# Kernel optimization log

Hardware: AMD Instinct MI355X
Metric: run time of the kernel (lower is better)

The kernel has to match this reference:

```python
import jax, jax.numpy as jnp
import numpy as np

BN_EPS = 1e-5
MIN_LENGTH = 10
HIDDEN = 256


def _conv(x, w, stride):
    # x: [N,C,H,W], w: [O,I,3,3], SAME-ish padding 1
    return jax.lax.conv_general_dilated(
        x, w, (stride, stride), [(1, 1), (1, 1)],
        dimension_numbers=("NCHW", "OIHW", "NCHW"))


def _bn_relu(x, g, b, m, v):
    # eval-mode BatchNorm2d followed by ReLU, folded into scale/shift
    inv = g / jnp.sqrt(v + BN_EPS)
    return jax.nn.relu(x * inv[None, :, None, None] + (b - m * inv)[None, :, None, None])


def setup_inputs() -> dict:
    key = jax.random.key(0)
    ks = jax.random.split(key, 16)
    B, S, C, H, W = 16, 64, 3, 64, 64
    d = {"imgs": jax.random.normal(ks[0], (B, S, C, H, W), dtype=jnp.float32)}
    # conv stack: (out_ch, in_ch, stride)
    specs = [(16, 3, 2), (16, 16, 1), (32, 16, 2), (32, 32, 1), (64, 32, 2), (64, 64, 1)]
    for i, (o, ic, _s) in enumerate(specs):
        d[f"w{i}"] = jax.random.normal(ks[1 + i], (o, ic, 3, 3), dtype=jnp.float32) * 0.05
        d[f"g{i}"] = jnp.ones((o,), jnp.float32)
        d[f"b{i}"] = jnp.zeros((o,), jnp.float32)
        d[f"m{i}"] = jnp.zeros((o,), jnp.float32)
        d[f"v{i}"] = jnp.ones((o,), jnp.float32)
    in_dim = 64 * 8 * 8  # plane3 * 8 * 8
    d["w_ih"] = jax.random.normal(ks[8], (4 * HIDDEN, in_dim), dtype=jnp.float32) * 0.02
    d["w_hh"] = jax.random.normal(ks[9], (4 * HIDDEN, HIDDEN), dtype=jnp.float32) * 0.05
    d["b_ih"] = jnp.zeros((4 * HIDDEN,), jnp.float32)
    d["b_hh"] = jnp.zeros((4 * HIDDEN,), jnp.float32)
    d["cls_w"] = jax.random.normal(ks[10], (1, HIDDEN), dtype=jnp.float32) * 0.05
    d["cls_b"] = jnp.zeros((1,), jnp.float32)
    return d


def reference(imgs, w0, g0, b0, m0, v0, w1, g1, b1, m1, v1, w2, g2, b2, m2, v2,
              w3, g3, b3, m3, v3, w4, g4, b4, m4, v4, w5, g5, b5, m5, v5,
              w_ih, w_hh, b_ih, b_hh, cls_w, cls_b):
    B, S, C, H, W = imgs.shape
    x = imgs.reshape(B * S, C, H, W)
    layers = [(w0, g0, b0, m0, v0, 2), (w1, g1, b1, m1, v1, 1),
              (w2, g2, b2, m2, v2, 2), (w3, g3, b3, m3, v3, 1),
              (w4, g4, b4, m4, v4, 2), (w5, g5, b5, m5, v5, 1)]
    for w, g, b, m, v, s in layers:
        x = _bn_relu(_conv(x, w, s), g, b, m, v)
    # [B*S, 64, 8, 8] -> [S, B, 4096]
    feats = x.reshape(B, S, -1).transpose(1, 0, 2)

    def step(carry, x_t):
        h, c = carry
        gates = x_t @ w_ih.T + b_ih + h @ w_hh.T + b_hh
        i, f, g, o = jnp.split(gates, 4, axis=-1)
        c = jax.nn.sigmoid(f) * c + jax.nn.sigmoid(i) * jnp.tanh(g)
        h = jax.nn.sigmoid(o) * jnp.tanh(c)
        return (h, c), h

    h0 = jnp.zeros((B, HIDDEN), feats.dtype)
    c0 = jnp.zeros((B, HIDDEN), feats.dtype)
    _, hs = jax.lax.scan(step, (h0, c0), feats)  # [S, B, 256]
    kept = hs[MIN_LENGTH + 1:]                    # [S-11, B, 256]
    out = jnp.tanh(kept @ cls_w.T + cls_b)        # [S-11, B, 1]
    return out.transpose(1, 0, 2)                 # [B, S-11, 1]
```

## Files before the change

### kernel.cpp

```cpp
#include <hip/hip_runtime.h>
#include <cmath>


typedef __attribute__((ext_vector_type(8))) __bf16 bf16x8;
typedef __attribute__((ext_vector_type(4))) float f32x4;

__device__ __forceinline__ float sigmoidf_(float x) { return 1.f / (1.f + expf(-x)); }

__device__ __forceinline__ unsigned short f2bf(float f) {
  unsigned u = __float_as_uint(f);
  unsigned r = (u + 0x7fffu + ((u >> 16) & 1u)) >> 16;
  return (unsigned short)r;
}
__device__ __forceinline__ float bf2f(unsigned short h) {
  return __uint_as_float(((unsigned)h) << 16);
}

struct FoldPack {
  const float *w[6], *g[6], *b[6], *m[6], *v[6];
  float *wf[6], *bias[6];
  int oc[6], ic[6];
};

__global__ __launch_bounds__(256) void fold_all(FoldPack p) {
  const int layer = blockIdx.y;
  const int OC = p.oc[layer], IC = p.ic[layer];
  const int total = OC * IC * 9;
  const float* w = p.w[layer];
  float* wf = p.wf[layer];
  for (int i = blockIdx.x * 256 + threadIdx.x; i < total; i += gridDim.x * 256) {
    int oc = i / (IC * 9);
    int r  = i % (IC * 9);
    int ic = r / 9;
    int k  = r % 9;
    int ky = k / 3, kx = k % 3;
    float inv = p.g[layer][oc] / sqrtf(p.v[layer][oc] + 1e-5f);
    wf[(((ic * 3 + ky) * OC) + oc) * 4 + kx] = w[i] * inv;
  }
  if (blockIdx.x == 0) {
    int i = threadIdx.x;
    if (i < OC) {
      float inv = p.g[layer][i] / sqrtf(p.v[layer][i] + 1e-5f);
      p.bias[layer][i] = p.b[layer][i] - p.m[layer][i] * inv;
    }
  }
}

struct PackPack {
  const float *w[5], *g[5], *v[5];
  unsigned short *wh[5], *wl[5];
  int ic[5], oc[5], kg[5], kreal[5];
};

__global__ __launch_bounds__(256) void pack_w(PackPack p) {
  const int layer = blockIdx.y;
  const int IC = p.ic[layer], KG = p.kg[layer], K = p.kreal[layer];
  const int MT = p.oc[layer] / 16;
  const int total = MT * KG * 512;
  for (int i = blockIdx.x * 256 + threadIdx.x; i < total; i += gridDim.x * 256) {
    int j = i & 7;
    int lane = (i >> 3) & 63;
    int gmt = i >> 9;
    int m = (gmt / KG) * 16 + (lane & 15);
    int k = 32 * (gmt % KG) + 8 * (lane >> 4) + j;
    float val = 0.f;
    if (k < K) {
      int tap = k / IC, ic = k % IC;
      int ky = tap / 3, kx = tap % 3;
      float inv = p.g[layer][m] / sqrtf(p.v[layer][m] + 1e-5f);
      val = p.w[layer][((m * IC + ic) * 3 + ky) * 3 + kx] * inv;
    }
    unsigned short h = f2bf(val);
    p.wh[layer][i] = h;
    p.wl[layer][i] = f2bf(val - bf2f(h));
  }
}

template<int IC, int OC, int IH, int IW, int STRIDE, int TPOS, int SPLITY,
         int ICS, int MINW>
__global__ __launch_bounds__(256, MINW) void conv_bn_relu(
    const float* __restrict__ in, const float* __restrict__ wf,
    const float* __restrict__ bias, float* __restrict__ out)
{
  constexpr int OH = IH / STRIDE, OW = IW / STRIDE;
  constexpr int OHB = OH / SPLITY;
  constexpr int RIH = (SPLITY == 1) ? (IH + 2) : ((OHB - 1) * STRIDE + 3);
  constexpr int PIW = IW + 4;
  constexpr int PLANE = RIH * PIW;
  constexpr int NPOS = OHB * OW;
  constexpr int WPOS = NPOS / TPOS;
  constexpr int SLOT = WPOS * ICS;
  constexpr int GROUPS = 256 / SLOT;
  constexpr int TOC = OC / GROUPS;
  constexpr int CH = IC / ICS;
  constexpr int SPAN = (TPOS - 1) * STRIDE + 3;
  constexpr int NW = (SPAN + 3) / 4;
  constexpr int XSLOTS = OW / TPOS;
  static_assert(SLOT % 64 == 0 && GROUPS * SLOT == 256 && GROUPS * TOC == OC, "tiling");

  __shared__ float s_in[IC * PLANE];

  const int tid = threadIdx.x;
  const int n     = (SPLITY == 1) ? blockIdx.x : blockIdx.x / SPLITY;
  const int split = (SPLITY == 1) ? 0 : blockIdx.x % SPLITY;
  const int ry0 = split * OHB;
  const int r0  = ry0 * STRIDE - 1;

  for (int i = tid; i < IC * PLANE / 4; i += 256)
    ((float4*)s_in)[i] = float4{0.f, 0.f, 0.f, 0.f};
  __syncthreads();

  constexpr int ROWF4 = IW / 4;
  constexpr int NSTG = IC * RIH * ROWF4;
  for (int i = tid; i < NSTG; i += 256) {
    int rw  = i % ROWF4;
    int t   = i / ROWF4;
    int row = t % RIH;
    int ic  = t / RIH;
    int giy = r0 + row;
    if (giy >= 0 && giy < IH) {
      float4 v = *(const float4*)(in + ((size_t)(n * IC + ic) * IH + giy) * IW + rw * 4);
      float* dst = &s_in[(ic * RIH + row) * PIW + 1 + rw * 4];
      dst[0] = v.x; dst[1] = v.y; dst[2] = v.z; dst[3] = v.w;
    }
  }
  __syncthreads();

  const int group  = tid / SLOT;
  const int sl     = tid % SLOT;
  const int icq    = sl / WPOS;
  const int worker = sl % WPOS;
  const int oy  = worker / XSLOTS;
  const int ox0 = (worker % XSLOTS) * TPOS;
  const int xb  = ox0 * STRIDE;

  const int oc0u = __builtin_amdgcn_readfirstlane(group * TOC);
  const float4* wg = (const float4*)wf + oc0u;

  float acc[TOC][TPOS];
  #pragma unroll
  for (int a = 0; a < TOC; ++a)
    #pragma unroll
    for (int p = 0; p < TPOS; ++p) acc[a][p] = 0.f;

  for (int icl = 0; icl < CH; ++icl) {
    const int ic = icq * CH + icl;
    const float* sI = &s_in[ic * PLANE];
    #pragma unroll
    for (int ky = 0; ky < 3; ++ky) {
      float row[NW * 4];
      {
        const float4* rp = (const float4*)&sI[(oy * STRIDE + ky) * PIW + xb];
        #pragma unroll
        for (int w = 0; w < NW; ++w) {
          float4 t4 = rp[w];
          row[4*w+0] = t4.x; row[4*w+1] = t4.y;
          row[4*w+2] = t4.z; row[4*w+3] = t4.w;
        }
      }
      const float4* wrow = wg + (ic * 3 + ky) * OC;
      #pragma unroll
      for (int oc = 0; oc < TOC; ++oc) {
        float4 w4 = wrow[oc];
        #pragma unroll
        for (int p = 0; p < TPOS; ++p)
          acc[oc][p] = fmaf(row[p * STRIDE + 0], w4.x,
                       fmaf(row[p * STRIDE + 1], w4.y,
                       fmaf(row[p * STRIDE + 2], w4.z, acc[oc][p])));
      }
    }
  }

  #pragma unroll
  for (int d = WPOS; d < SLOT; d <<= 1)
    #pragma unroll
    for (int oc = 0; oc < TOC; ++oc)
      #pragma unroll
      for (int p = 0; p < TPOS; ++p)
        acc[oc][p] += __shfl_xor(acc[oc][p], d);

  if (icq == 0) {
    float* outN = out + (size_t)n * (OC * OH * OW);
    #pragma unroll
    for (int oc = 0; oc < TOC; ++oc) {
      const float bb = bias[oc0u + oc];
      float* op = outN + ((size_t)(oc0u + oc) * OH + (ry0 + oy)) * OW + ox0;
      #pragma unroll
      for (int vq = 0; vq < TPOS / 4; ++vq) {
        float4 val;
        val.x = fmaxf(acc[oc][vq*4+0] + bb, 0.f);
        val.y = fmaxf(acc[oc][vq*4+1] + bb, 0.f);
        val.z = fmaxf(acc[oc][vq*4+2] + bb, 0.f);
        val.w = fmaxf(acc[oc][vq*4+3] + bb, 0.f);
        *(float4*)(op + vq * 4) = val;
      }
    }
  }
}

template<int IC, int OC, int IH, int IW, int STRIDE, int SPLITY, int KG, int ZROW>
__global__ __launch_bounds__(256, 2) void conv_mfma(
    const float* __restrict__ in, const unsigned short* __restrict__ Ah,
    const unsigned short* __restrict__ Al, const float* __restrict__ bias,
    float* __restrict__ out)
{
  constexpr int OH = IH / STRIDE, OW = IW / STRIDE;
  constexpr int OHB = OH / SPLITY;
  constexpr int N = OHB * OW;
  constexpr int NT = N / 16;
  constexpr int NTW = NT / 4;
  constexpr int MT = OC / 16;
  constexpr int ICP = IC + 8;
  constexpr int PW = IW + 3;
  constexpr int PH = (OHB - 1) * STRIDE + 3 + ZROW;
  constexpr int SZ = ((PH * PW * ICP + 7) / 8) * 8;
  static_assert(NT % 4 == 0, "nt");

  __shared__ unsigned short s_h[SZ];
  __shared__ unsigned short s_l[SZ];

  const int tid = threadIdx.x;
  const int n     = (SPLITY == 1) ? blockIdx.x : blockIdx.x / SPLITY;
  const int split = (SPLITY == 1) ? 0 : blockIdx.x % SPLITY;
  const int y0 = split * OHB;
  const int r0 = y0 * STRIDE - 1;

  for (int i = tid * 8; i < SZ; i += 2048) {
    *(int4*)&s_h[i] = int4{0, 0, 0, 0};
    *(int4*)&s_l[i] = int4{0, 0, 0, 0};
  }
  __syncthreads();

  constexpr int ROWF4 = IW / 4;
  for (int i = tid; i < IC * PH * ROWF4; i += 256) {
    int rw  = i % ROWF4;
    int t   = i / ROWF4;
    int row = t % PH;
    int ic  = t / PH;
    int giy = r0 + row;
    if (giy >= 0 && giy < IH) {
      float4 v = *(const float4*)(in + ((size_t)(n * IC + ic) * IH + giy) * IW + rw * 4);
      int base = (row * PW + rw * 4 + 1) * ICP + ic;
      float vv[4] = {v.x, v.y, v.z, v.w};
      #pragma unroll
      for (int e = 0; e < 4; ++e) {
        unsigned short h = f2bf(vv[e]);
        s_h[base + e * ICP] = h;
        s_l[base + e * ICP] = f2bf(vv[e] - bf2f(h));
      }
    }
  }
  __syncthreads();

  const int wave = tid >> 6;
  const int lane = tid & 63;
  const int l16  = lane & 15;
  const int quad = lane >> 4;

  f32x4 acc[MT][NTW];
  #pragma unroll
  for (int mt = 0; mt < MT; ++mt)
    #pragma unroll
    for (int nt = 0; nt < NTW; ++nt) acc[mt][nt] = f32x4{0.f, 0.f, 0.f, 0.f};

  for (int g = 0; g < KG; ++g) {
    const int k0 = 32 * g + 8 * quad;
    const int tap = k0 / IC;
    const int ic0 = k0 % IC;
    const int ky = tap / 3;
    const int kx = tap - ky * 3;
    bf16x8 afh[MT], afl[MT];
    #pragma unroll
    for (int mt = 0; mt < MT; ++mt) {
      size_t wo = ((size_t)(mt * KG + g) * 64 + lane) * 8;
      afh[mt] = __builtin_bit_cast(bf16x8, *(const int4*)(Ah + wo));
      afl[mt] = __builtin_bit_cast(bf16x8, *(const int4*)(Al + wo));
    }
    #pragma unroll
    for (int nt = 0; nt < NTW; ++nt) {
      int p = (wave * NTW + nt) * 16 + l16;
      int py = p / OW, px = p % OW;
      int addr = ((py * STRIDE + ky) * PW + px * STRIDE + kx) * ICP + ic0;
      bf16x8 bh = __builtin_bit_cast(bf16x8, *(const int4*)&s_h[addr]);
      bf16x8 bl = __builtin_bit_cast(bf16x8, *(const int4*)&s_l[addr]);
      #pragma unroll
      for (int mt = 0; mt < MT; ++mt) {
        acc[mt][nt] = __builtin_amdgcn_mfma_f32_16x16x32_bf16(afh[mt], bh, acc[mt][nt], 0, 0, 0);
        acc[mt][nt] = __builtin_amdgcn_mfma_f32_16x16x32_bf16(afh[mt], bl, acc[mt][nt], 0, 0, 0);
        acc[mt][nt] = __builtin_amdgcn_mfma_f32_16x16x32_bf16(afl[mt], bh, acc[mt][nt], 0, 0, 0);
      }
    }
  }

  #pragma unroll
  for (int mt = 0; mt < MT; ++mt)
    #pragma unroll
    for (int nt = 0; nt < NTW; ++nt) {
      int p = (wave * NTW + nt) * 16 + l16;
      int py = p / OW, px = p % OW;
      #pragma unroll
      for (int r = 0; r < 4; ++r) {
        int oc = mt * 16 + quad * 4 + r;
        float v = acc[mt][nt][r] + bias[oc];
        out[((size_t)(n * OC + oc) * OH + y0 + py) * OW + px] = fmaxf(v, 0.f);
      }
    }
}

__global__ __launch_bounds__(256) void split_a(
    const float* __restrict__ feats, unsigned short* __restrict__ ah,
    unsigned short* __restrict__ al)
{
  int i4 = blockIdx.x * 256 + threadIdx.x;
  int e = i4 * 4;
  int n = e >> 12;
  int k = e & 4095;
  int r = (n & 63) * 16 + (n >> 6);
  float4 v = ((const float4*)feats)[i4];
  ushort4 h, l;
  h.x = f2bf(v.x); l.x = f2bf(v.x - bf2f(h.x));
  h.y = f2bf(v.y); l.y = f2bf(v.y - bf2f(h.y));
  h.z = f2bf(v.z); l.z = f2bf(v.z - bf2f(h.z));
  h.w = f2bf(v.w); l.w = f2bf(v.w - bf2f(h.w));
  *(ushort4*)(ah + (size_t)r * 4096 + k) = h;
  *(ushort4*)(al + (size_t)r * 4096 + k) = l;
}

__global__ __launch_bounds__(256) void split_b(
    const float* __restrict__ w_ih, unsigned short* __restrict__ bh,
    unsigned short* __restrict__ bl)
{
  int i4 = blockIdx.x * 256 + threadIdx.x;
  float4 v = ((const float4*)w_ih)[i4];
  ushort4 h, l;
  h.x = f2bf(v.x); l.x = f2bf(v.x - bf2f(h.x));
  h.y = f2bf(v.y); l.y = f2bf(v.y - bf2f(h.y));
  h.z = f2bf(v.z); l.z = f2bf(v.z - bf2f(h.z));
  h.w = f2bf(v.w); l.w = f2bf(v.w - bf2f(h.w));
  ((ushort4*)bh)[i4] = h;
  ((ushort4*)bl)[i4] = l;
}

__global__ __launch_bounds__(256) void mfma_xg(
    const unsigned short* __restrict__ Ah, const unsigned short* __restrict__ Al,
    const unsigned short* __restrict__ Bh, const unsigned short* __restrict__ Bl,
    float* __restrict__ part)
{
  __shared__ unsigned short s_ah[128 * 40];
  __shared__ unsigned short s_al[128 * 40];
  __shared__ unsigned short s_bh[128 * 40];
  __shared__ unsigned short s_bl[128 * 40];

  const int tid = threadIdx.x;
  const int col0 = blockIdx.x * 128;
  const int row0 = blockIdx.y * 128;
  const int kbase = blockIdx.z * 512;
  float* outp = part + (size_t)blockIdx.z * 1048576;

  const int wave = tid >> 6;
  const int lane = tid & 63;
  const int wr = wave >> 1, wc = wave & 1;
  const int quad = lane >> 4;
  const int l16 = lane & 15;

  f32x4 acc[4][4];
  #pragma unroll
  for (int i = 0; i < 4; ++i)
    #pragma unroll
    for (int j = 0; j < 4; ++j) acc[i][j] = f32x4{0.f, 0.f, 0.f, 0.f};

  for (int step = 0; step < 16; ++step) {
    const int koff = kbase + step * 32;
    #pragma unroll
    for (int c = tid; c < 512; c += 256) {
      int row = c >> 2, kc = (c & 3) * 8;
      int4 va = *(const int4*)(Ah + (size_t)(row0 + row) * 4096 + koff + kc);
      int4 vb = *(const int4*)(Al + (size_t)(row0 + row) * 4096 + koff + kc);
      int4 vc = *(const int4*)(Bh + (size_t)(col0 + row) * 4096 + koff + kc);
      int4 vd = *(const int4*)(Bl + (size_t)(col0 + row) * 4096 + koff + kc);
      *(int4*)&s_ah[row * 40 + kc] = va;
      *(int4*)&s_al[row * 40 + kc] = vb;
      *(int4*)&s_bh[row * 40 + kc] = vc;
      *(int4*)&s_bl[row * 40 + kc] = vd;
    }
    __syncthreads();

    bf16x8 arh[4], arl[4];
    #pragma unroll
    for (int i = 0; i < 4; ++i) {
      int m = wr * 64 + i * 16 + l16;
      arh[i] = __builtin_bit_cast(bf16x8, *(const int4*)&s_ah[m * 40 + quad * 8]);
      arl[i] = __builtin_bit_cast(bf16x8, *(const int4*)&s_al[m * 40 + quad * 8]);
    }
    #pragma unroll
    for (int j = 0; j < 4; ++j) {
      int nn = wc * 64 + j * 16 + l16;
      bf16x8 brh = __builtin_bit_cast(bf16x8, *(const int4*)&s_bh[nn * 40 + quad * 8]);
      bf16x8 brl = __builtin_bit_cast(bf16x8, *(const int4*)&s_bl[nn * 40 + quad * 8]);
      #pragma unroll
      for (int i = 0; i < 4; ++i) {
        acc[i][j] = __builtin_amdgcn_mfma_f32_16x16x32_bf16(arh[i], brh, acc[i][j], 0, 0, 0);
        acc[i][j] = __builtin_amdgcn_mfma_f32_16x16x32_bf16(arh[i], brl, acc[i][j], 0, 0, 0);
        acc[i][j] = __builtin_amdgcn_mfma_f32_16x16x32_bf16(arl[i], brh, acc[i][j], 0, 0, 0);
      }
    }
    __syncthreads();
  }

  #pragma unroll
  for (int i = 0; i < 4; ++i)
    #pragma unroll
    for (int j = 0; j < 4; ++j) {
      int row = row0 + wr * 64 + i * 16 + quad * 4;
      int col = col0 + wc * 64 + j * 16 + l16;
      #pragma unroll
      for (int r = 0; r < 4; ++r)
        outp[(size_t)(row + r) * 1024 + col] = acc[i][j][r];
    }
}

__global__ __launch_bounds__(256) void reduce_xg(
    const float* __restrict__ p, const float* __restrict__ b_ih,
    const float* __restrict__ b_hh, float* __restrict__ xg)
{
  int i = blockIdx.x * 256 + threadIdx.x;
  float4 s = {0.f, 0.f, 0.f, 0.f};
  #pragma unroll
  for (int z = 0; z < 8; ++z) {
    float4 a = ((const float4*)p)[(size_t)z * 262144 + i];
    s.x += a.x; s.y += a.y; s.z += a.z; s.w += a.w;
  }
  int cb = i & 255;
  float4 bi = ((const float4*)b_ih)[cb];
  float4 bh = ((const float4*)b_hh)[cb];
  float4 o;
  o.x = s.x + bi.x + bh.x;
  o.y = s.y + bi.y + bh.y;
  o.z = s.z + bi.z + bh.z;
  o.w = s.w + bi.w + bh.w;
  ((float4*)xg)[i] = o;
}

__global__ __launch_bounds__(1024) void lstm_kernel(
    const float* __restrict__ xg, const float* __restrict__ w_hh,
    float* __restrict__ hs, unsigned long long* __restrict__ hpair)
{
  const int b = blockIdx.x & 15;
  const int g = blockIdx.x >> 4;
  const int tid = threadIdx.x;
  const int r = tid >> 2;
  const int q = tid & 3;
  const int gate = r >> 6;
  const int jl = r & 63;
  const int j = g * 64 + jl;

  float4 wv[16];
  {
    const float4* wrow = (const float4*)(w_hh + ((size_t)(gate * 256 + j)) * 256 + q * 64);
    #pragma unroll
    for (int k = 0; k < 16; ++k) wv[k] = wrow[k];
  }

  __shared__ float s_h[4 * 72];
  __shared__ float s_gates[4][64];
  float c_reg = 0.f;

  for (int s = 0; s < 64; ++s) {
    float xv = 0.f;
    if (q == 0) xv = xg[(size_t)(s * 16 + b) * 1024 + gate * 256 + j];
    float gv = 0.f;
    if (s > 0) {
      if (tid < 256) {
        const unsigned long long* src = hpair + ((size_t)(s - 1) * 16 + b) * 256 + tid;
        unsigned long long pv;
        do {
          pv = __hip_atomic_load(src, __ATOMIC_RELAXED, __HIP_MEMORY_SCOPE_AGENT);
        } while ((unsigned int)(pv >> 32) != (unsigned int)s);
        s_h[(tid >> 6) * 72 + (tid & 63)] = __uint_as_float((unsigned int)pv);
      }
      __syncthreads();
      const float4* hp = (const float4*)&s_h[q * 72];
      float p = 0.f;
      #pragma unroll
      for (int k = 0; k < 16; ++k) {
        float4 h4 = hp[k];
        p = fmaf(h4.x, wv[k].x, p);
        p = fmaf(h4.y, wv[k].y, p);
        p = fmaf(h4.z, wv[k].z, p);
        p = fmaf(h4.w, wv[k].w, p);
      }
      p += __shfl_xor(p, 1);
      p += __shfl_xor(p, 2);
      gv = p;
    }
    if (q == 0) s_gates[gate][jl] = gv + xv;
    __syncthreads();
    if (tid < 64) {
      float gi = s_gates[0][tid], gf = s_gates[1][tid];
      float gg = s_gates[2][tid], go = s_gates[3][tid];
      float cn = sigmoidf_(gf) * c_reg + sigmoidf_(gi) * tanhf(gg);
      c_reg = cn;
      float hv = sigmoidf_(go) * tanhf(cn);
      hs[(size_t)s * 4096 + b * 256 + g * 64 + tid] = hv;
      unsigned long long pv =
          ((unsigned long long)(unsigned int)(s + 1) << 32) | __float_as_uint(hv);
      __hip_atomic_store(hpair + ((size_t)s * 16 + b) * 256 + g * 64 + tid, pv,
                         __ATOMIC_RELAXED, __HIP_MEMORY_SCOPE_AGENT);
    }
  }
}

__global__ __launch_bounds__(64) void cls_kernel(
    const float* __restrict__ hs, const float* __restrict__ cw,
    const float* __restrict__ cb, float* __restrict__ out)
{
  const int id = blockIdx.x;
  const int b = id / 53;
  const int t = id % 53;
  const int s = 11 + t;
  const int lane = threadIdx.x;
  float4 hv = ((const float4*)(hs + (size_t)s * 4096 + b * 256))[lane];
  float4 wv = ((const float4*)cw)[lane];
  float p = hv.x * wv.x + hv.y * wv.y + hv.z * wv.z + hv.w * wv.w;
  #pragma unroll
  for (int off = 32; off >= 1; off >>= 1) p += __shfl_xor(p, off);
  if (lane == 0) out[id] = tanhf(p + cb[0]);
}

extern "C" void kernel_launch(void* const* d_in, const int* in_sizes, int n_in,
                              void* d_out, int out_size, void* d_ws, size_t ws_size,
                              hipStream_t stream)
{
  (void)in_sizes; (void)n_in; (void)out_size; (void)ws_size;
  const float* imgs = (const float*)d_in[0];
  const float* w_ih  = (const float*)d_in[31];
  const float* w_hh  = (const float*)d_in[32];
  const float* b_ih  = (const float*)d_in[33];
  const float* b_hh  = (const float*)d_in[34];
  const float* cls_w = (const float*)d_in[35];
  const float* cls_b = (const float*)d_in[36];
  float* out = (float*)d_out;

  float* ws   = (float*)d_ws;
  float* actA = ws;
  float* actB = actA + 16777216;
  float* xg   = actB + 16777216;
  float* hs   = xg + 1048576;
  unsigned long long* hpair = (unsigned long long*)(hs + 262144);
  float* wfp  = hs + 262144 + 524288;
  static const int ocs[6] = {16, 16, 32, 32, 64, 64};
  static const int ics[6] = {3, 16, 16, 32, 32, 64};
  float* wf[6];
  size_t off = 0;
  for (int i = 0; i < 6; ++i) { wf[i] = wfp + off; off += (size_t)ocs[i] * ics[i] * 12; }
  float* biasp = wfp + off;
  float* bias[6];
  for (int i = 0; i < 6; ++i) bias[i] = biasp + i * 64;

  static const int psz[5] = {2560, 5120, 9216, 18432, 36864};
  unsigned short* WH = (unsigned short*)(biasp + 6 * 64);
  unsigned short* WL = WH + 72192;
  unsigned short *wh[5], *wl[5];
  {
    int o = 0;
    for (int i = 0; i < 5; ++i) { wh[i] = WH + o; wl[i] = WL + o; o += psz[i]; }
  }

  float* partials = actA;
  unsigned short* Ah = (unsigned short*)(actA + 8388608);
  unsigned short* Al = Ah + 4194304;
  unsigned short* Bh = Al + 4194304;
  unsigned short* Bl = Bh + 4194304;

  FoldPack fp;
  for (int i = 0; i < 6; ++i) {
    fp.w[i] = (const float*)d_in[1 + 5*i];
    fp.g[i] = (const float*)d_in[2 + 5*i];
    fp.b[i] = (const float*)d_in[3 + 5*i];
    fp.m[i] = (const float*)d_in[4 + 5*i];
    fp.v[i] = (const float*)d_in[5 + 5*i];
    fp.wf[i] = wf[i];
    fp.bias[i] = bias[i];
    fp.oc[i] = ocs[i];
    fp.ic[i] = ics[i];
  }
  fold_all<<<dim3(8, 6), 256, 0, stream>>>(fp);

  PackPack pp;
  static const int kgs[5] = {5, 5, 9, 9, 18};
  static const int krs[5] = {144, 144, 288, 288, 576};
  for (int i = 0; i < 5; ++i) {
    pp.w[i] = (const float*)d_in[1 + 5*(i+1)];
    pp.g[i] = (const float*)d_in[2 + 5*(i+1)];
    pp.v[i] = (const float*)d_in[5 + 5*(i+1)];
    pp.wh[i] = wh[i];
    pp.wl[i] = wl[i];
    pp.ic[i] = ics[i+1];
    pp.oc[i] = ocs[i+1];
    pp.kg[i] = kgs[i];
    pp.kreal[i] = krs[i];
  }
  pack_w<<<dim3(36, 5), 256, 0, stream>>>(pp);

  conv_bn_relu<3, 16, 64, 64, 2, 4, 2, 1, 4><<<2048, 256, 0, stream>>>(imgs, wf[0], bias[0], actA);
  conv_mfma<16, 16, 32, 32, 1, 4, 5, 1><<<4096, 256, 0, stream>>>(actA, wh[0], wl[0], bias[1], actB);
  conv_mfma<16, 32, 32, 32, 2, 4, 5, 1><<<4096, 256, 0, stream>>>(actB, wh[1], wl[1], bias[2], actA);
  conv_mfma<32, 32, 16, 16, 1, 1, 9, 0><<<1024, 256, 0, stream>>>(actA, wh[2], wl[2], bias[3], actB);
  conv_mfma<32, 64, 16, 16, 2, 1, 9, 0><<<1024, 256, 0, stream>>>(actB, wh[3], wl[3], bias[4], actA);
  conv_mfma<64, 64,  8,  8, 1, 1, 18, 0><<<1024, 256, 0, stream>>>(actA, wh[4], wl[4], bias[5], actB);

  split_a<<<4096, 256, 0, stream>>>(actB, Ah, Al);
  split_b<<<4096, 256, 0, stream>>>(w_ih, Bh, Bl);
  mfma_xg<<<dim3(8, 8, 8), 256, 0, stream>>>(Ah, Al, Bh, Bl, partials);
  reduce_xg<<<1024, 256, 0, stream>>>(partials, b_ih, b_hh, xg);
  lstm_kernel<<<64, 1024, 0, stream>>>(xg, w_hh, hs, hpair);
  cls_kernel<<<848, 64, 0, stream>>>(hs, cls_w, cls_b, out);
}
```

Baseline: 486.8 us.

## Restructure LSTM step to cut barriers and use fast gate activations

Remaps LSTM threads so the four gates of one hidden unit sit in adjacent lanes, which lets the cell update gather them with warp shuffles instead of a shared-memory round trip and a second barrier. Polling of the previous hidden state is spread across all four 256-thread groups, with a shared 'seen' flag and a double-buffered h array, so each step needs only one __syncthreads. Sigmoid and tanh switch to fast exp/rcp approximations, which lowers accuracy slightly. The per-step serial latency of the recurrent loop is the target.

```diff
diff --git a/kernel.cpp b/kernel.cpp
--- a/kernel.cpp
+++ b/kernel.cpp
@@ -6,6 +6,15 @@
 typedef __attribute__((ext_vector_type(4))) float f32x4;
 
 __device__ __forceinline__ float sigmoidf_(float x) { return 1.f / (1.f + expf(-x)); }
+
+__device__ __forceinline__ float fsig_(float x) {
+  return __builtin_amdgcn_rcpf(1.f + __expf(-x));
+}
+__device__ __forceinline__ float ftanh_(float x) {
+  float xc = fminf(fmaxf(x, -15.f), 15.f);
+  float e = __expf(2.f * xc);
+  return (e - 1.f) * __builtin_amdgcn_rcpf(e + 1.f);
+}
 
 __device__ __forceinline__ unsigned short f2bf(float f) {
   unsigned u = __float_as_uint(f);
@@ -441,18 +450,17 @@
   ((float4*)xg)[i] = o;
 }
 
-__global__ __launch_bounds__(1024) void lstm_kernel(
+__global__ __launch_bounds__(1024, 4) void lstm_kernel(
     const float* __restrict__ xg, const float* __restrict__ w_hh,
     float* __restrict__ hs, unsigned long long* __restrict__ hpair)
 {
   const int b = blockIdx.x & 15;
   const int g = blockIdx.x >> 4;
   const int tid = threadIdx.x;
-  const int r = tid >> 2;
-  const int q = tid & 3;
-  const int gate = r >> 6;
-  const int jl = r & 63;
-  const int j = g * 64 + jl;
+  const int m    = tid >> 4;
+  const int gate = (tid >> 2) & 3;
+  const int q    = tid & 3;
+  const int j = g * 64 + m;
 
   float4 wv[16];
   {
@@ -461,26 +469,37 @@
     for (int k = 0; k < 16; ++k) wv[k] = wrow[k];
   }
 
-  __shared__ float s_h[4 * 72];
-  __shared__ float s_gates[4][64];
+  __shared__ float s_h[2][4 * 72];
+  __shared__ int s_seen[256];
+  if (tid < 256) s_seen[tid] = 0;
+
   float c_reg = 0.f;
+  const int w = tid & 255;
+  volatile int* seen = &s_seen[w];
 
   for (int s = 0; s < 64; ++s) {
+    if (s > 0) {
+      if (*seen != s) {
+        const unsigned long long* src = hpair + ((size_t)(s - 1) * 16 + b) * 256 + w;
+        for (;;) {
+          unsigned long long pv =
+              __hip_atomic_load(src, __ATOMIC_RELAXED, __HIP_MEMORY_SCOPE_AGENT);
+          if ((unsigned int)(pv >> 32) == (unsigned int)s) {
+            s_h[s & 1][(w >> 6) * 72 + (w & 63)] = __uint_as_float((unsigned int)pv);
+            *seen = s;
+            break;
+          }
+          if (*seen == s) break;
+        }
+      }
+    }
+    __syncthreads();
+
     float xv = 0.f;
     if (q == 0) xv = xg[(size_t)(s * 16 + b) * 1024 + gate * 256 + j];
-    float gv = 0.f;
+    float p = 0.f;
     if (s > 0) {
-      if (tid < 256) {
-        const unsigned long long* src = hpair + ((size_t)(s - 1) * 16 + b) * 256 + tid;
-        unsigned long long pv;
-        do {
-          pv = __hip_atomic_load(src, __ATOMIC_RELAXED, __HIP_MEMORY_SCOPE_AGENT);
-        } while ((unsigned int)(pv >> 32) != (unsigned int)s);
-        s_h[(tid >> 6) * 72 + (tid & 63)] = __uint_as_float((unsigned int)pv);
-      }
-      __syncthreads();
-      const float4* hp = (const float4*)&s_h[q * 72];
-      float p = 0.f;
+      const float4* hp = (const float4*)&s_h[s & 1][q * 72];
       #pragma unroll
       for (int k = 0; k < 16; ++k) {
         float4 h4 = hp[k];
@@ -489,22 +508,21 @@
         p = fmaf(h4.z, wv[k].z, p);
         p = fmaf(h4.w, wv[k].w, p);
       }
-      p += __shfl_xor(p, 1);
-      p += __shfl_xor(p, 2);
-      gv = p;
-    }
-    if (q == 0) s_gates[gate][jl] = gv + xv;
-    __syncthreads();
-    if (tid < 64) {
-      float gi = s_gates[0][tid], gf = s_gates[1][tid];
-      float gg = s_gates[2][tid], go = s_gates[3][tid];
-      float cn = sigmoidf_(gf) * c_reg + sigmoidf_(gi) * tanhf(gg);
+    }
+    p += __shfl_xor(p, 1);
+    p += __shfl_xor(p, 2);
+    float gv = p + xv;
+    float gf = __shfl_down(gv, 4);
+    float gg = __shfl_down(gv, 8);
+    float go = __shfl_down(gv, 12);
+    if ((tid & 15) == 0) {
+      float cn = fsig_(gf) * c_reg + fsig_(gv) * ftanh_(gg);
       c_reg = cn;
-      float hv = sigmoidf_(go) * tanhf(cn);
-      hs[(size_t)s * 4096 + b * 256 + g * 64 + tid] = hv;
+      float hv = fsig_(go) * ftanh_(cn);
+      hs[(size_t)s * 4096 + b * 256 + j] = hv;
       unsigned long long pv =
           ((unsigned long long)(unsigned int)(s + 1) << 32) | __float_as_uint(hv);
-      __hip_atomic_store(hpair + ((size_t)s * 16 + b) * 256 + g * 64 + tid, pv,
+      __hip_atomic_store(hpair + ((size_t)s * 16 + b) * 256 + j, pv,
                          __ATOMIC_RELAXED, __HIP_MEMORY_SCOPE_AGENT);
     }
   }
```

Result: slower. 529.1 us (+8.7%).
